# Kernel optimization log

Hardware: AMD Instinct MI355X
Metric: run time of the kernel (lower is better)

The kernel has to match this reference:

```python
import jax, jax.numpy as jnp
import numpy as np

EPS = 1e-12


def setup_inputs() -> dict:
    key = jax.random.key(0)
    k1, k2 = jax.random.split(key)
    B, P, D = 8, 4096, 2
    pred = jax.random.normal(k1, (B, P, D), dtype=jnp.float32)
    gt = jax.random.normal(k2, (B, P, D), dtype=jnp.float32)
    return {"pred": pred, "gt": gt}


def reference(pred, gt):
    # cdist(p=2): ||a||^2 + ||b||^2 - 2 a.b, clamped, sqrt  -> [B, P, P]
    p2 = jnp.sum(pred * pred, axis=-1)          # [B, P]
    g2 = jnp.sum(gt * gt, axis=-1)               # [B, P]
    cross = jnp.einsum("bnd,bmd->bnm", pred, gt)  # [B, P, P]
    d2 = p2[:, :, None] + g2[:, None, :] - 2.0 * cross
    matrix = jnp.sqrt(jnp.maximum(d2, EPS))      # [B, P_pred, P_gt]
    pred2gt_min = jnp.min(matrix, axis=1)        # min over pred index, per gt point
    gt2pred_min = jnp.min(matrix, axis=2)        # min over gt index, per pred point
    return 0.5 * (jnp.mean(pred2gt_min) + jnp.mean(gt2pred_min))
```

## Files before the change

### kernel.cpp

```cpp
#include <hip/hip_runtime.h>


#define NB    8
#define NP    4096
#define XBINS 2048
#define W     0.0048828125f
#define XMIN  -5.0f
#define INVW  204.8f
#define BSSTR (XBINS + 4)
#define WH    128

__device__ __forceinline__ int xbin(float x) {
    int i = (int)((x - XMIN) * INVW);
    return i < 0 ? 0 : (i > XBINS - 1 ? XBINS - 1 : i);
}

__global__ __launch_bounds__(256) void xSort(const float* __restrict__ pred,
                                             const float* __restrict__ gt,
                                             float2* __restrict__ P,
                                             unsigned* __restrict__ BS,
                                             float* __restrict__ out) {
    __shared__ unsigned cnt[XBINS];
    __shared__ unsigned waveTot[4];

    int t = threadIdx.x;
    int s = blockIdx.x;
    int b = s >> 1, side = s & 1;

    if (s == 0 && t == 0) *out = 0.0f;

    const float2* src = (const float2*)(side ? gt : pred) + (size_t)b * NP;
    float2*   dst = P  + (size_t)s * NP;
    unsigned* bs  = BS + (size_t)s * BSSTR;

#pragma unroll
    for (int i = 0; i < XBINS / 256; ++i) cnt[t * (XBINS / 256) + i] = 0;
    __syncthreads();

    for (int i = t; i < NP; i += 256)
        atomicAdd(&cnt[xbin(src[i].x)], 1u);
    __syncthreads();

    unsigned local = 0;
#pragma unroll
    for (int i = 0; i < XBINS / 256; ++i) local += cnt[t * (XBINS / 256) + i];

    unsigned inc = local;
#pragma unroll
    for (int o = 1; o < 64; o <<= 1) {
        unsigned n = __shfl_up(inc, o, 64);
        if ((t & 63) >= o) inc += n;
    }
    if ((t & 63) == 63) waveTot[t >> 6] = inc;
    __syncthreads();
    unsigned wbase = 0;
#pragma unroll
    for (int w = 0; w < 4; ++w) if (w < (t >> 6)) wbase += waveTot[w];
    unsigned run = wbase + inc - local;

#pragma unroll
    for (int i = 0; i < XBINS / 256; ++i) {
        unsigned c = cnt[t * (XBINS / 256) + i];
        cnt[t * (XBINS / 256) + i] = run;
        run += c;
    }
    __syncthreads();

    for (int i = t; i < XBINS; i += 256) bs[i] = cnt[i];
    if (t == 0) bs[XBINS] = NP;
    __syncthreads();

    for (int i = t; i < NP; i += 256) {
        float2 p = src[i];
        unsigned pos = atomicAdd(&cnt[xbin(p.x)], 1u);
        dst[pos] = p;
    }
}

__global__ __launch_bounds__(256) void winSearch(const float2* __restrict__ P,
                                                 const unsigned* __restrict__ BS,
                                                 float* __restrict__ out) {
    __shared__ __align__(16) float2 sp[NP];
    __shared__ __align__(16) unsigned short sbs[XBINS];

    int t     = threadIdx.x;
    int bid   = blockIdx.x;
    int qs    = bid & 15;
    int slice = bid >> 4;
    int b = qs & 7, dir = qs >> 3;

    int tgt = b * 2 + (1 - dir);
    const float2*   tp = P  + (size_t)tgt * NP;
    const unsigned* bs = BS + (size_t)tgt * BSSTR;

    const float4* tp4 = (const float4*)tp;
    float4*       sp4w = (float4*)sp;
#pragma unroll
    for (int i = 0; i < 8; ++i) sp4w[t + i * 256] = tp4[t + i * 256];
    const uint4* bs4  = (const uint4*)bs;
    uint2*       sbs2 = (uint2*)sbs;
#pragma unroll
    for (int i = 0; i < 2; ++i) {
        uint4 v = bs4[t + i * 256];
        sbs2[t + i * 256] = make_uint2(v.x | (v.y << 16), v.z | (v.w << 16));
    }

    const float2* qarr = P + (size_t)(b * 2 + dir) * NP;
    float2 q = qarr[slice * 256 + t];
    __syncthreads();

    float qx = q.x, qy = q.y;
    int r0 = (int)sbs[xbin(qx)];

    int w0 = r0 - WH;
    if (w0 < 0) w0 = 0;
    if (w0 > NP - 2 * WH) w0 = NP - 2 * WH;
    w0 &= ~1;

    float best = 3.402823466e+38f;
    const float4* spc = (const float4*)sp;
    int base = w0 >> 1;
#pragma unroll 8
    for (int k = 0; k < WH; ++k) {
        float4 v = spc[base + k];
        float dx0 = qx - v.x, dy0 = qy - v.y;
        float dx1 = qx - v.z, dy1 = qy - v.w;
        float d0 = fmaf(dx0, dx0, dy0 * dy0);
        float d1 = fmaf(dx1, dx1, dy1 * dy1);
        best = fminf(fminf(best, d0), d1);
    }

    float lbL = (w0 > 0)          ? fmaxf(qx - sp[w0].x - W, 0.0f)              : 3.0e38f;
    float lbR = (w0 + 2 * WH < NP) ? fmaxf(sp[w0 + 2 * WH - 1].x - W - qx, 0.0f) : 3.0e38f;
    bool uncert = (lbL * lbL < best) || (lbR * lbR < best);

    unsigned long long mask = __ballot(uncert);
    int lane = t & 63;
    while (mask) {
        int l = __ffsll((long long)mask) - 1;
        mask &= mask - 1;
        float qlx = __shfl(qx, l, 64);
        float qly = __shfl(qy, l, 64);
        float rb = 3.402823466e+38f;
#pragma unroll 4
        for (int i = 0; i < 32; ++i) {
            float4 v = spc[lane + i * 64];
            float dx0 = qlx - v.x, dy0 = qly - v.y;
            float dx1 = qlx - v.z, dy1 = qly - v.w;
            rb = fminf(rb, fmaf(dx0, dx0, dy0 * dy0));
            rb = fminf(rb, fmaf(dx1, dx1, dy1 * dy1));
        }
#pragma unroll
        for (int o = 32; o > 0; o >>= 1) rb = fminf(rb, __shfl_xor(rb, o, 64));
        if (lane == l) best = rb;
    }

    float v = sqrtf(fmaxf(best, 1e-12f));

#pragma unroll
    for (int o = 32; o > 0; o >>= 1) v += __shfl_down(v, o, 64);

    __shared__ float wsum[4];
    if ((t & 63) == 0) wsum[t >> 6] = v;
    __syncthreads();
    if (t == 0)
        atomicAdd(out, ((wsum[0] + wsum[1]) + (wsum[2] + wsum[3])) *
                           (0.5f / (float)(NB * NP)));
}

extern "C" void kernel_launch(void* const* d_in, const int* in_sizes, int n_in,
                              void* d_out, int out_size, void* d_ws, size_t ws_size,
                              hipStream_t stream) {
    const float* pred = (const float*)d_in[0];
    const float* gt   = (const float*)d_in[1];
    float*       out  = (float*)d_out;

    float2*   P  = (float2*)d_ws;
    unsigned* BS = (unsigned*)(P + (size_t)16 * NP);

    (void)in_sizes; (void)n_in; (void)out_size; (void)ws_size;

    xSort<<<16, 256, 0, stream>>>(pred, gt, P, BS, out);
    winSearch<<<256, 256, 0, stream>>>(P, BS, out);
}
```

Baseline: 25.87 us.

## Fuse sort and window search into one kernel with per-block LDS sort

Replaces the two-kernel pipeline (global counting sort into workspace, then window search) with one kernel. Each block counting-sorts its target cloud directly into LDS and locally sorts its 256 queries by x-bin so that lanes in a wave hit nearby windows. This removes the global workspace round trip and the dependency between a 16-block kernel and the search kernel. In exchange, every one of the 256 blocks redoes the sort of its 4096 target points, and a small zeroing kernel is added.

```diff
diff --git a/kernel.cpp b/kernel.cpp
--- a/kernel.cpp
+++ b/kernel.cpp
@@ -7,7 +7,6 @@
 #define W     0.0048828125f
 #define XMIN  -5.0f
 #define INVW  204.8f
-#define BSSTR (XBINS + 4)
 #define WH    128
 
 __device__ __forceinline__ int xbin(float x) {
@@ -15,36 +14,46 @@
     return i < 0 ? 0 : (i > XBINS - 1 ? XBINS - 1 : i);
 }
 
-__global__ __launch_bounds__(256) void xSort(const float* __restrict__ pred,
-                                             const float* __restrict__ gt,
-                                             float2* __restrict__ P,
-                                             unsigned* __restrict__ BS,
-                                             float* __restrict__ out) {
-    __shared__ unsigned cnt[XBINS];
+__global__ void zeroOut(float* __restrict__ out) {
+    if (threadIdx.x == 0) *out = 0.0f;
+}
+
+#define FOREACH8(M) M(0) M(1) M(2) M(3) M(4) M(5) M(6) M(7)
+
+__global__ __launch_bounds__(256) void sortSearch(const float* __restrict__ pred,
+                                                  const float* __restrict__ gt,
+                                                  float* __restrict__ out) {
+    __shared__ __align__(16) float2 sp[NP];
+    __shared__ __align__(16) unsigned cnt[XBINS];
+    __shared__ __align__(16) float2 qs2[256];
+    __shared__ __align__(8)  unsigned short jb[256];
+    __shared__ float wsum[4];
     __shared__ unsigned waveTot[4];
 
-    int t = threadIdx.x;
-    int s = blockIdx.x;
-    int b = s >> 1, side = s & 1;
+    int t     = threadIdx.x;
+    int bid   = blockIdx.x;
+    int qs    = bid & 15;
+    int slice = bid >> 4;
+    int b = qs & 7, dir = qs >> 3;
 
-    if (s == 0 && t == 0) *out = 0.0f;
-
-    const float2* src = (const float2*)(side ? gt : pred) + (size_t)b * NP;
-    float2*   dst = P  + (size_t)s * NP;
-    unsigned* bs  = BS + (size_t)s * BSSTR;
+    const float2* tp = (const float2*)(dir ? pred : gt) + (size_t)b * NP;
+    const float2* qp = (const float2*)(dir ? gt : pred) + (size_t)b * NP;
 
 #pragma unroll
-    for (int i = 0; i < XBINS / 256; ++i) cnt[t * (XBINS / 256) + i] = 0;
+    for (int i = 0; i < XBINS / 256; ++i) cnt[t + i * 256] = 0;
+    float2 myq = qp[slice * 256 + t];
     __syncthreads();
 
-    for (int i = t; i < NP; i += 256)
-        atomicAdd(&cnt[xbin(src[i].x)], 1u);
+    const float4* tp4 = (const float4*)tp;
+#define DECLV(i) float4 v##i = tp4[t + (i) * 256]; \
+    atomicAdd(&cnt[xbin(v##i.x)], 1u); atomicAdd(&cnt[xbin(v##i.z)], 1u);
+    FOREACH8(DECLV)
+#undef DECLV
     __syncthreads();
 
     unsigned local = 0;
 #pragma unroll
-    for (int i = 0; i < XBINS / 256; ++i) local += cnt[t * (XBINS / 256) + i];
-
+    for (int i = 0; i < 8; ++i) local += cnt[t * 8 + i];
     unsigned inc = local;
 #pragma unroll
     for (int o = 1; o < 64; o <<= 1) {
@@ -57,60 +66,45 @@
 #pragma unroll
     for (int w = 0; w < 4; ++w) if (w < (t >> 6)) wbase += waveTot[w];
     unsigned run = wbase + inc - local;
-
 #pragma unroll
-    for (int i = 0; i < XBINS / 256; ++i) {
-        unsigned c = cnt[t * (XBINS / 256) + i];
-        cnt[t * (XBINS / 256) + i] = run;
+    for (int i = 0; i < 8; ++i) {
+        unsigned c = cnt[t * 8 + i];
+        cnt[t * 8 + i] = run;
         run += c;
     }
     __syncthreads();
 
-    for (int i = t; i < XBINS; i += 256) bs[i] = cnt[i];
-    if (t == 0) bs[XBINS] = NP;
+#define SCAT(i) { \
+    unsigned p0 = atomicAdd(&cnt[xbin(v##i.x)], 1u); \
+    sp[p0] = (float2){v##i.x, v##i.y}; \
+    unsigned p1 = atomicAdd(&cnt[xbin(v##i.z)], 1u); \
+    sp[p1] = (float2){v##i.z, v##i.w}; }
+    FOREACH8(SCAT)
+#undef SCAT
+
+    int j = xbin(myq.x);
+    jb[t] = (unsigned short)j;
     __syncthreads();
+    int rank = 0;
+    const uint2* jbp = (const uint2*)jb;
+#pragma unroll 8
+    for (int kk = 0; kk < 64; ++kk) {
+        uint2 w2 = jbp[kk];
+        int k0 = kk * 4;
+        int j0 = w2.x & 0xffff, j1 = w2.x >> 16;
+        int j2 = w2.y & 0xffff, j3 = w2.y >> 16;
+        rank += (j0 < j) || (j0 == j && k0 < t);
+        rank += (j1 < j) || (j1 == j && k0 + 1 < t);
+        rank += (j2 < j) || (j2 == j && k0 + 2 < t);
+        rank += (j3 < j) || (j3 == j && k0 + 3 < t);
+    }
+    qs2[rank] = myq;
+    __syncthreads();
+    myq = qs2[t];
+    float qx = myq.x, qy = myq.y;
 
-    for (int i = t; i < NP; i += 256) {
-        float2 p = src[i];
-        unsigned pos = atomicAdd(&cnt[xbin(p.x)], 1u);
-        dst[pos] = p;
-    }
-}
-
-__global__ __launch_bounds__(256) void winSearch(const float2* __restrict__ P,
-                                                 const unsigned* __restrict__ BS,
-                                                 float* __restrict__ out) {
-    __shared__ __align__(16) float2 sp[NP];
-    __shared__ __align__(16) unsigned short sbs[XBINS];
-
-    int t     = threadIdx.x;
-    int bid   = blockIdx.x;
-    int qs    = bid & 15;
-    int slice = bid >> 4;
-    int b = qs & 7, dir = qs >> 3;
-
-    int tgt = b * 2 + (1 - dir);
-    const float2*   tp = P  + (size_t)tgt * NP;
-    const unsigned* bs = BS + (size_t)tgt * BSSTR;
-
-    const float4* tp4 = (const float4*)tp;
-    float4*       sp4w = (float4*)sp;
-#pragma unroll
-    for (int i = 0; i < 8; ++i) sp4w[t + i * 256] = tp4[t + i * 256];
-    const uint4* bs4  = (const uint4*)bs;
-    uint2*       sbs2 = (uint2*)sbs;
-#pragma unroll
-    for (int i = 0; i < 2; ++i) {
-        uint4 v = bs4[t + i * 256];
-        sbs2[t + i * 256] = make_uint2(v.x | (v.y << 16), v.z | (v.w << 16));
-    }
-
-    const float2* qarr = P + (size_t)(b * 2 + dir) * NP;
-    float2 q = qarr[slice * 256 + t];
-    __syncthreads();
-
-    float qx = q.x, qy = q.y;
-    int r0 = (int)sbs[xbin(qx)];
+    int jq = xbin(qx);
+    int r0 = (jq == 0) ? 0 : (int)cnt[jq - 1];
 
     int w0 = r0 - WH;
     if (w0 < 0) w0 = 0;
@@ -130,8 +124,8 @@
         best = fminf(fminf(best, d0), d1);
     }
 
-    float lbL = (w0 > 0)          ? fmaxf(qx - sp[w0].x - W, 0.0f)              : 3.0e38f;
-    float lbR = (w0 + 2 * WH < NP) ? fmaxf(sp[w0 + 2 * WH - 1].x - W - qx, 0.0f) : 3.0e38f;
+    float lbL = (w0 > 0)           ? fmaxf(qx - sp[w0].x - W, 0.0f)               : 3.0e38f;
+    float lbR = (w0 + 2 * WH < NP) ? fmaxf(sp[w0 + 2 * WH - 1].x - W - qx, 0.0f)  : 3.0e38f;
     bool uncert = (lbL * lbL < best) || (lbR * lbR < best);
 
     unsigned long long mask = __ballot(uncert);
@@ -156,11 +150,8 @@
     }
 
     float v = sqrtf(fmaxf(best, 1e-12f));
-
 #pragma unroll
     for (int o = 32; o > 0; o >>= 1) v += __shfl_down(v, o, 64);
-
-    __shared__ float wsum[4];
     if ((t & 63) == 0) wsum[t >> 6] = v;
     __syncthreads();
     if (t == 0)
@@ -175,11 +166,8 @@
     const float* gt   = (const float*)d_in[1];
     float*       out  = (float*)d_out;
 
-    float2*   P  = (float2*)d_ws;
-    unsigned* BS = (unsigned*)(P + (size_t)16 * NP);
+    (void)in_sizes; (void)n_in; (void)out_size; (void)d_ws; (void)ws_size;
 
-    (void)in_sizes; (void)n_in; (void)out_size; (void)ws_size;
-
-    xSort<<<16, 256, 0, stream>>>(pred, gt, P, BS, out);
-    winSearch<<<256, 256, 0, stream>>>(P, BS, out);
+    zeroOut<<<1, 64, 0, stream>>>(out);
+    sortSearch<<<256, 256, 0, stream>>>(pred, gt, out);
 }
```

New measurement: 33.45 us. +29.3%, slower.
